# Kernel tuning notes

Hardware: AMD Instinct MI355X
Metric: run time of the kernel (lower is better)

Reference implementation:

```python
import jax, jax.numpy as jnp
import numpy as np

B, S, D, H = 2, 2048, 1024, 16
DH = D // H
NEG = -1000000000.0


def setup_inputs() -> dict:
    key = jax.random.key(0)
    ks = jax.random.split(key, 8)
    q = jax.random.normal(ks[0], (B, S, D), dtype=jnp.float32)
    k = jax.random.normal(ks[1], (B, S, D), dtype=jnp.float32)
    v = jax.random.normal(ks[2], (B, S, D), dtype=jnp.float32)
    # padding mask [B, k_len]; ensure first key position is valid
    mask = jax.random.randint(ks[3], (B, S), 0, 2, dtype=jnp.int32)
    mask = mask.at[:, 0].set(1)
    scale = 1.0 / np.sqrt(D)
    Wq = jax.random.normal(ks[4], (D, D), dtype=jnp.float32) * scale
    Wk = jax.random.normal(ks[5], (D, D), dtype=jnp.float32) * scale
    Wv = jax.random.normal(ks[6], (D, D), dtype=jnp.float32) * scale
    Wo = jax.random.normal(ks[7], (D, D), dtype=jnp.float32) * scale
    return {"q": q, "k": k, "v": v, "mask": mask,
            "Wq": Wq, "Wk": Wk, "Wv": Wv, "Wo": Wo}


def reference(q, k, v, mask, Wq, Wk, Wv, Wo):
    # nn.Linear(bias=False): y = x @ W.T  (W is [out, in])
    Q = jnp.einsum('bsd,ed->bse', q, Wq)
    K = jnp.einsum('bsd,ed->bse', k, Wk)
    V = jnp.einsum('bsd,ed->bse', v, Wv)
    # split heads -> [B, H, S, DH]
    Q = Q.reshape(B, S, H, DH).transpose(0, 2, 1, 3)
    K = K.reshape(B, S, H, DH).transpose(0, 2, 1, 3)
    V = V.reshape(B, S, H, DH).transpose(0, 2, 1, 3)
    scores = jnp.einsum('bhqd,bhkd->bhqk', Q, K) / jnp.float32(np.sqrt(DH))
    # padding mask: [B, K] -> additive [B, 1, 1, K]
    pad = jnp.where(mask == 0, jnp.float32(NEG), jnp.float32(0.0))[:, None, None, :]
    scores = scores + pad
    # causal (mask_future=True): strict upper triangle blocked
    causal = jnp.where(jnp.triu(jnp.ones((S, S), dtype=bool), k=1),
                       jnp.float32(NEG), jnp.float32(0.0))
    scores = scores + causal
    attn = jax.nn.softmax(scores, axis=-1)
    out = jnp.einsum('bhqk,bhkd->bhqd', attn, V)  # [B, H, S, DH]
    out = out.transpose(0, 2, 1, 3).reshape(B, S, D)
    out = jnp.einsum('bsd,ed->bse', out, Wo)
    # dropout: identity in eval mode
    return out
```

## Files before the change

### kernel.cpp

```cpp
#include <hip/hip_runtime.h>
#include <stdint.h>

#define BB 2
#define SS 2048
#define DD 1024
#define HH 16
#define DHH 64

typedef __bf16 bf16_t;
typedef bf16_t bf16x8 __attribute__((ext_vector_type(8)));
typedef float f32x4 __attribute__((ext_vector_type(4)));
typedef short s16x4 __attribute__((ext_vector_type(4)));

union FragU { uint4 u; bf16x8 b; };
union Frag4U { uint2 u; s16x4 s; };

#if __has_builtin(__builtin_amdgcn_exp2f)
#define EXP2(x) __builtin_amdgcn_exp2f(x)
#else
#define EXP2(x) exp2f(x)
#endif

__device__ __forceinline__ unsigned short f2bf(float f) {
  union { float f; unsigned int u; } x; x.f = f;
  unsigned int u = x.u;
  return (unsigned short)((u + 0x7FFFu + ((u >> 16) & 1u)) >> 16);
}

__device__ __forceinline__ uint2 pack4(float4 v) {
  uint2 r;
  r.x = (unsigned)f2bf(v.x) | ((unsigned)f2bf(v.y) << 16);
  r.y = (unsigned)f2bf(v.z) | ((unsigned)f2bf(v.w) << 16);
  return r;
}

__device__ __forceinline__ uint2 packAcc(f32x4 a) {
  uint2 r;
  r.x = (unsigned)f2bf(a[0]) | ((unsigned)f2bf(a[1]) << 16);
  r.y = (unsigned)f2bf(a[2]) | ((unsigned)f2bf(a[3]) << 16);
  return r;
}

__device__ __forceinline__ bf16x8 ldsFrag(const unsigned short* s, int idx) {
  FragU f;
  f.u = *reinterpret_cast<const uint4*>(s + idx);
  return f.b;
}

__device__ __forceinline__ void gload_lds16(const unsigned short* g, unsigned short* s) {
  __builtin_amdgcn_global_load_lds(
      (const __attribute__((address_space(1))) unsigned int*)g,
      (__attribute__((address_space(3))) unsigned int*)s, 16, 0, 0);
}

#define MFMA16(a, b, c) __builtin_amdgcn_mfma_f32_16x16x32_bf16((a), (b), (c), 0, 0, 0)
#define MFMA16K16(a, b, c) __builtin_amdgcn_mfma_f32_16x16x16bf16_1k((a), (b), (c), 0, 0, 0)

__global__ __launch_bounds__(256) void convert_kernel(
    const float* __restrict__ q, const float* __restrict__ k, const float* __restrict__ v,
    const float* __restrict__ Wq, const float* __restrict__ Wk,
    const float* __restrict__ Wv, const float* __restrict__ Wo,
    const int* __restrict__ mask,
    unsigned short* __restrict__ Ab, unsigned short* __restrict__ Wb,
    float* __restrict__ Mf) {
  const int z = blockIdx.y;
  if (z == 7) {
    if (blockIdx.x >= 4) return;
    const size_t base = (size_t)blockIdx.x * 1024 + (size_t)threadIdx.x * 4;
    int4 m4 = *reinterpret_cast<const int4*>(mask + base);
    float4 p;
    p.x = (m4.x == 0) ? -1.0e9f : 0.0f;
    p.y = (m4.y == 0) ? -1.0e9f : 0.0f;
    p.z = (m4.z == 0) ? -1.0e9f : 0.0f;
    p.w = (m4.w == 0) ? -1.0e9f : 0.0f;
    *reinterpret_cast<float4*>(Mf + base) = p;
    return;
  }
  const float* src;
  unsigned short* dst;
  float scale = 1.0f;
  if (z < 3) {
    src = (z == 0) ? q : (z == 1) ? k : v;
    dst = Ab + (size_t)z * BB * SS * DD;
  } else {
    if (blockIdx.x >= (DD * DD / 1024)) return;
    src = (z == 3) ? Wq : (z == 4) ? Wk : (z == 5) ? Wv : Wo;
    dst = Wb + (size_t)(z - 3) * DD * DD;
    if (z == 3) scale = 0.125f * 1.44269504088896f;
  }
  const size_t base = (size_t)blockIdx.x * 1024 + (size_t)threadIdx.x * 4;
  float4 val = *reinterpret_cast<const float4*>(src + base);
  val.x *= scale; val.y *= scale; val.z *= scale; val.w *= scale;
  uint2 p = pack4(val);
  *reinterpret_cast<uint2*>(dst + base) = p;
}

__global__ __launch_bounds__(256) void proj128_kernel(
    const unsigned short* __restrict__ Ab, const unsigned short* __restrict__ Wb,
    unsigned short* __restrict__ Qb, unsigned short* __restrict__ Kb,
    unsigned short* __restrict__ Vt) {
  __shared__ unsigned short sA[2][128 * 64];
  __shared__ unsigned short sB[2][128 * 64];

  const int z = blockIdx.z;
  const unsigned short* A = Ab + (size_t)z * BB * SS * DD;
  const unsigned short* W = Wb + (size_t)z * DD * DD;
  unsigned short* Out = (z == 0) ? Qb : (z == 1) ? Kb : Vt;
  const int layout = (z == 2) ? 1 : 0;

  const int t = threadIdx.x;
  const int lane = t & 63, wave = t >> 6;
  const int quad = lane >> 4, l15 = lane & 15;
  const int wr = wave >> 1, wc = wave & 1;
  const int mBase = blockIdx.x * 128, nBase = blockIdx.y * 128;
  const int srow = lane >> 3, soct = lane & 7;

  f32x4 acc[4][4] = {};

  #pragma unroll
  for (int i = 0; i < 4; ++i) {
    const int g = wave * 4 + i;
    const int row = g * 8 + srow;
    const int oct = soct ^ (row & 7);
    gload_lds16(A + (size_t)(mBase + row) * DD + oct * 8, &sA[0][g * 512]);
    gload_lds16(W + (size_t)(nBase + row) * DD + oct * 8, &sB[0][g * 512]);
  }

  for (int kt = 0; kt < DD / 64; ++kt) {
    __syncthreads();
    if (kt + 1 < DD / 64) {
      const int nb = (kt + 1) & 1;
      const int k1 = (kt + 1) * 64;
      #pragma unroll
      for (int i = 0; i < 4; ++i) {
        const int g = wave * 4 + i;
        const int row = g * 8 + srow;
        const int oct = soct ^ (row & 7);
        gload_lds16(A + (size_t)(mBase + row) * DD + k1 + oct * 8, &sA[nb][g * 512]);
        gload_lds16(W + (size_t)(nBase + row) * DD + k1 + oct * 8, &sB[nb][g * 512]);
      }
    }
    const int cb = kt & 1;
    #pragma unroll
    for (int kk = 0; kk < 2; ++kk) {
      bf16x8 af[4], bfr[4];
      #pragma unroll
      for (int i = 0; i < 4; ++i) {
        const int row = wr * 64 + i * 16 + l15;
        af[i] = ldsFrag(sA[cb], (row * 8 + ((kk * 4 + quad) ^ (l15 & 7))) * 8);
      }
      #pragma unroll
      for (int j = 0; j < 4; ++j) {
        const int row = wc * 64 + j * 16 + l15;
        bfr[j] = ldsFrag(sB[cb], (row * 8 + ((kk * 4 + quad) ^ (l15 & 7))) * 8);
      }
      if (layout == 0) {
        #pragma unroll
        for (int i = 0; i < 4; ++i)
          #pragma unroll
          for (int j = 0; j < 4; ++j)
            acc[i][j] = MFMA16(bfr[j], af[i], acc[i][j]);
      } else {
        #pragma unroll
        for (int i = 0; i < 4; ++i)
          #pragma unroll
          for (int j = 0; j < 4; ++j)
            acc[i][j] = MFMA16(af[i], bfr[j], acc[i][j]);
      }
    }
  }

  const int b = mBase >> 11;
  const int sbase = mBase & (SS - 1);
  if (layout == 0) {
    #pragma unroll
    for (int i = 0; i < 4; ++i) {
      #pragma unroll
      for (int j = 0; j < 4; ++j) {
        const int s = sbase + wr * 64 + i * 16 + l15;
        const int n = nBase + wc * 64 + j * 16 + quad * 4;
        const int h = n >> 6, dh = n & (DHH - 1);
        uint2 w = packAcc(acc[i][j]);
        *reinterpret_cast<uint2*>(
            Out + ((size_t)(b * HH + h) * SS + s) * DHH + dh) = w;
      }
    }
  } else {
    #pragma unroll
    for (int i = 0; i < 4; ++i) {
      #pragma unroll
      for (int j = 0; j < 4; ++j) {
        const int s = sbase + wr * 64 + i * 16 + quad * 4;
        const int n = nBase + wc * 64 + j * 16 + l15;
        const int h = n >> 6, dh = n & (DHH - 1);
        uint2 w = packAcc(acc[i][j]);
        *reinterpret_cast<uint2*>(
            Out + ((size_t)(b * HH + h) * DHH + dh) * SS + s) = w;
      }
    }
  }
}

__global__ __launch_bounds__(256, 4) void attn_kernel(
    const unsigned short* __restrict__ Qb, const unsigned short* __restrict__ Kb,
    const unsigned short* __restrict__ Vt, const float* __restrict__ Mf,
    unsigned short* __restrict__ Obh) {
  __shared__ __align__(16) unsigned short sK[2][64 * 64];
  __shared__ __align__(16) unsigned short sV[2][64 * 64];
  unsigned short* sO = &sK[0][0];

  const int t = threadIdx.x;
  const int lane = t & 63, wave = t >> 6;
  const int quad = lane >> 4, l15 = lane & 15;

  const int id = blockIdx.x;
  const int xcd = id & 7, rest = id >> 3;
  const int hg = rest >> 5;
  const int hd = xcd * 4 + hg;
  const int r5 = rest & 31;
  const int qt = (hg & 1) ? (31 - r5) : r5;
  const int b = hd >> 4;
  const int qb = qt * 64;

  const size_t headOff = (size_t)hd * SS * DHH;
  const unsigned short* Qh = Qb + headOff;
  const unsigned short* Kh = Kb + headOff;
  const unsigned short* Vh = Vt + headOff;
  const float* Mp = Mf + b * SS;

  bf16x8 aq[2];
  {
    const unsigned short* qp = Qh + (size_t)(qb + wave * 16 + l15) * DHH + quad * 8;
    FragU f0, f1;
    f0.u = *reinterpret_cast<const uint4*>(qp);
    f1.u = *reinterpret_cast<const uint4*>(qp + 32);
    aq[0] = f0.b; aq[1] = f1.b;
  }

  const int srow = lane >> 3, soct = lane & 7;

  #pragma unroll
  for (int i = 0; i < 2; ++i) {
    const int g = wave * 2 + i;
    const int row = g * 8 + srow;
    const int oct = soct ^ (row & 7);
    gload_lds16(Kh + (size_t)row * DHH + oct * 8, &sK[0][g * 512]);
    gload_lds16(Vh + (size_t)row * SS + oct * 8, &sV[0][g * 512]);
  }

  float l_lane = 0.0f;
  f32x4 oacc[4] = {};
  const int qrow_abs = qb + wave * 16 + l15;

  for (int c = 0; c <= qt; ++c) {
    __syncthreads();
    if (c < qt) {
      const int c1 = (c + 1) * 64;
      const int nb = (c + 1) & 1;
      #pragma unroll
      for (int i = 0; i < 2; ++i) {
        const int g = wave * 2 + i;
        const int row = g * 8 + srow;
        const int oct = soct ^ (row & 7);
        gload_lds16(Kh + (size_t)(c1 + row) * DHH + oct * 8, &sK[nb][g * 512]);
        gload_lds16(Vh + (size_t)row * SS + c1 + oct * 8, &sV[nb][g * 512]);
      }
    }
    const int cb = c & 1;
    const int c0 = c * 64;

    f32x4 sacc[4] = {};
    #pragma unroll
    for (int kk = 0; kk < 2; ++kk) {
      #pragma unroll
      for (int j = 0; j < 4; ++j) {
        const int row = j * 16 + l15;
        bf16x8 ak = ldsFrag(sK[cb], (row * 8 + ((kk * 4 + quad) ^ (l15 & 7))) * 8);
        sacc[j] = MFMA16(ak, aq[kk], sacc[j]);
      }
    }

    const bool diag = (c == qt);
    s16x4 pk[4];
    #pragma unroll
    for (int j = 0; j < 4; ++j) {
      float4 pf = *reinterpret_cast<const float4*>(Mp + c0 + j * 16 + quad * 4);
      float p0 = EXP2(sacc[j][0] + pf.x);
      float p1 = EXP2(sacc[j][1] + pf.y);
      float p2 = EXP2(sacc[j][2] + pf.z);
      float p3 = EXP2(sacc[j][3] + pf.w);
      if (diag) {
        const int key = c0 + j * 16 + quad * 4;
        p0 = (key + 0 > qrow_abs) ? 0.0f : p0;
        p1 = (key + 1 > qrow_abs) ? 0.0f : p1;
        p2 = (key + 2 > qrow_abs) ? 0.0f : p2;
        p3 = (key + 3 > qrow_abs) ? 0.0f : p3;
      }
      l_lane += (p0 + p1) + (p2 + p3);
      Frag4U fu;
      fu.u.x = __builtin_amdgcn_perm(__float_as_uint(p1) + 0x8000u,
                                     __float_as_uint(p0) + 0x8000u, 0x07060302u);
      fu.u.y = __builtin_amdgcn_perm(__float_as_uint(p3) + 0x8000u,
                                     __float_as_uint(p2) + 0x8000u, 0x07060302u);
      pk[j] = fu.s;
    }

    #pragma unroll
    for (int j = 0; j < 4; ++j) {
      #pragma unroll
      for (int jn = 0; jn < 4; ++jn) {
        const int row = jn * 16 + l15;
        const int oct = (2 * j + (quad >> 1)) ^ (l15 & 7);
        Frag4U av;
        av.u = *reinterpret_cast<const uint2*>(&sV[cb][(row * 8 + oct) * 8 + (quad & 1) * 4]);
        oacc[jn] = MFMA16K16(av.s, pk[j], oacc[jn]);
      }
    }
  }

  float l_l = l_lane + __shfl_xor(l_lane, 16);
  l_l += __shfl_xor(l_l, 32);
  __syncthreads();
  const float inv = 1.0f / l_l;
  #pragma unroll
  for (int jn = 0; jn < 4; ++jn) {
    uint2 w;
    w.x = (unsigned)f2bf(oacc[jn][0] * inv) | ((unsigned)f2bf(oacc[jn][1] * inv) << 16);
    w.y = (unsigned)f2bf(oacc[jn][2] * inv) | ((unsigned)f2bf(oacc[jn][3] * inv) << 16);
    *reinterpret_cast<uint2*>(&sO[(wave * 16 + l15) * 72 + jn * 16 + quad * 4]) = w;
  }
  __syncthreads();
  {
    const int row = t >> 2, seg = t & 3;
    uint4 u0 = *reinterpret_cast<const uint4*>(&sO[row * 72 + seg * 16]);
    uint4 u1 = *reinterpret_cast<const uint4*>(&sO[row * 72 + seg * 16 + 8]);
    unsigned short* dst = Obh + headOff + (size_t)(qb + row) * DHH + seg * 16;
    *reinterpret_cast<uint4*>(dst) = u0;
    *reinterpret_cast<uint4*>(dst + 8) = u1;
  }
}

__global__ __launch_bounds__(256) void outproj_kernel(
    const unsigned short* __restrict__ Obh, const unsigned short* __restrict__ Wb,
    float* __restrict__ Out) {
  __shared__ unsigned short sA[2][128 * 64];
  __shared__ unsigned short sB[2][128 * 64];

  const unsigned short* W = Wb + (size_t)3 * DD * DD;
  const int t = threadIdx.x;
  const int lane = t & 63, wave = t >> 6;
  const int quad = lane >> 4, l15 = lane & 15;
  const int wr = wave >> 1, wc = wave & 1;
  const int mBase = blockIdx.x * 128, nBase = blockIdx.y * 128;
  const int srow = lane >> 3, soct = lane & 7;

  const int bidx = mBase >> 11;
  const int sloc = mBase & (SS - 1);
  const unsigned short* Abase = Obh + (size_t)bidx * HH * SS * DHH;

  f32x4 acc[4][4] = {};

  #pragma unroll
  for (int i = 0; i < 4; ++i) {
    const int g = wave * 4 + i;
    const int row = g * 8 + srow;
    const int oct = soct ^ (row & 7);
    gload_lds16(Abase + ((size_t)0 * SS + sloc + row) * DHH + oct * 8, &sA[0][g * 512]);
    gload_lds16(W + (size_t)(nBase + row) * DD + oct * 8, &sB[0][g * 512]);
  }

  for (int kt = 0; kt < HH; ++kt) {
    __syncthreads();
    if (kt + 1 < HH) {
      const int nb = (kt + 1) & 1;
      #pragma unroll
      for (int i = 0; i < 4; ++i) {
        const int g = wave * 4 + i;
        const int row = g * 8 + srow;
        const int oct = soct ^ (row & 7);
        gload_lds16(Abase + ((size_t)(kt + 1) * SS + sloc + row) * DHH + oct * 8,
                    &sA[nb][g * 512]);
        gload_lds16(W + (size_t)(nBase + row) * DD + (kt + 1) * 64 + oct * 8,
                    &sB[nb][g * 512]);
      }
    }
    const int cb = kt & 1;
    #pragma unroll
    for (int kk = 0; kk < 2; ++kk) {
      bf16x8 af[4], bfr[4];
      #pragma unroll
      for (int i = 0; i < 4; ++i) {
        const int row = wr * 64 + i * 16 + l15;
        af[i] = ldsFrag(sA[cb], (row * 8 + ((kk * 4 + quad) ^ (l15 & 7))) * 8);
      }
      #pragma unroll
      for (int j = 0; j < 4; ++j) {
        const int row = wc * 64 + j * 16 + l15;
        bfr[j] = ldsFrag(sB[cb], (row * 8 + ((kk * 4 + quad) ^ (l15 & 7))) * 8);
      }
      #pragma unroll
      for (int i = 0; i < 4; ++i)
        #pragma unroll
        for (int j = 0; j < 4; ++j)
          acc[i][j] = MFMA16(bfr[j], af[i], acc[i][j]);
    }
  }

  #pragma unroll
  for (int i = 0; i < 4; ++i) {
    #pragma unroll
    for (int j = 0; j < 4; ++j) {
      const int m = mBase + wr * 64 + i * 16 + l15;
      const int n = nBase + wc * 64 + j * 16 + quad * 4;
      float4 w;
      w.x = acc[i][j][0]; w.y = acc[i][j][1];
      w.z = acc[i][j][2]; w.w = acc[i][j][3];
      *reinterpret_cast<float4*>(Out + (size_t)m * DD + n) = w;
    }
  }
}

extern "C" void kernel_launch(void* const* d_in, const int* in_sizes, int n_in,
                              void* d_out, int out_size, void* d_ws, size_t ws_size,
                              hipStream_t stream) {
  (void)in_sizes; (void)n_in; (void)out_size; (void)ws_size;
  const float* q  = (const float*)d_in[0];
  const float* k  = (const float*)d_in[1];
  const float* v  = (const float*)d_in[2];
  const int* mask = (const int*)d_in[3];
  const float* Wq = (const float*)d_in[4];
  const float* Wk = (const float*)d_in[5];
  const float* Wv = (const float*)d_in[6];
  const float* Wo = (const float*)d_in[7];
  float* out = (float*)d_out;

  const size_t AE = (size_t)BB * SS * DD;
  unsigned short* Ab  = (unsigned short*)d_ws;
  unsigned short* Obh = Ab;
  unsigned short* Wb  = Ab + 3 * AE;
  unsigned short* Qb  = Wb + (size_t)4 * DD * DD;
  unsigned short* Kb  = Qb + AE;
  unsigned short* Vt  = Kb + AE;
  float* Mf = (float*)(Vt + AE);

  convert_kernel<<<dim3(AE / 1024, 8), 256, 0, stream>>>(
      q, k, v, Wq, Wk, Wv, Wo, mask, Ab, Wb, Mf);

  proj128_kernel<<<dim3(BB * SS / 128, DD / 128, 3), 256, 0, stream>>>(
      Ab, Wb, Qb, Kb, Vt);

  attn_kernel<<<dim3(32 * HH * BB), 256, 0, stream>>>(Qb, Kb, Vt, Mf, Obh);

  outproj_kernel<<<dim3(BB * SS / 128, DD / 128), 256, 0, stream>>>(Obh, Wb, out);
}
```

Baseline: 224.5 us.

## Process two 64-row query subtiles per attention block to reuse K/V tiles

Each attention block now handles 128 query rows as two 64-row subtiles that share every staged K/V chunk and its LDS fragment loads. This halves the grid and the global K/V traffic per query row. The padding mask row is also preloaded into shared memory instead of being read from global memory per chunk. In exchange, register pressure roughly doubles, occupancy is reduced to 2 blocks per SIMD, fewer blocks are available for load balancing, and the diagonal chunks need special-case masking.

```diff
diff --git a/kernel.cpp b/kernel.cpp
--- a/kernel.cpp
+++ b/kernel.cpp
@@ -201,12 +201,13 @@
   }
 }
 
-__global__ __launch_bounds__(256, 4) void attn_kernel(
+__global__ __launch_bounds__(256, 2) void attn_kernel(
     const unsigned short* __restrict__ Qb, const unsigned short* __restrict__ Kb,
     const unsigned short* __restrict__ Vt, const float* __restrict__ Mf,
     unsigned short* __restrict__ Obh) {
   __shared__ __align__(16) unsigned short sK[2][64 * 64];
   __shared__ __align__(16) unsigned short sV[2][64 * 64];
+  __shared__ __align__(16) float sM[SS];
   unsigned short* sO = &sK[0][0];
 
   const int t = threadIdx.x;
@@ -215,12 +216,12 @@
 
   const int id = blockIdx.x;
   const int xcd = id & 7, rest = id >> 3;
-  const int hg = rest >> 5;
+  const int hg = rest >> 4;
   const int hd = xcd * 4 + hg;
-  const int r5 = rest & 31;
-  const int qt = (hg & 1) ? (31 - r5) : r5;
+  const int r4 = rest & 15;
+  const int qtl = (hg & 2) ? (15 - r4) : r4;
   const int b = hd >> 4;
-  const int qb = qt * 64;
+  const int qb = qtl * 128;
 
   const size_t headOff = (size_t)hd * SS * DHH;
   const unsigned short* Qh = Qb + headOff;
@@ -228,16 +229,25 @@
   const unsigned short* Vh = Vt + headOff;
   const float* Mp = Mf + b * SS;
 
-  bf16x8 aq[2];
-  {
-    const unsigned short* qp = Qh + (size_t)(qb + wave * 16 + l15) * DHH + quad * 8;
+  bf16x8 aq[2][2];
+  #pragma unroll
+  for (int sub = 0; sub < 2; ++sub) {
+    const unsigned short* qp =
+        Qh + (size_t)(qb + sub * 64 + wave * 16 + l15) * DHH + quad * 8;
     FragU f0, f1;
     f0.u = *reinterpret_cast<const uint4*>(qp);
     f1.u = *reinterpret_cast<const uint4*>(qp + 32);
-    aq[0] = f0.b; aq[1] = f1.b;
+    aq[sub][0] = f0.b; aq[sub][1] = f1.b;
   }
 
   const int srow = lane >> 3, soct = lane & 7;
+
+  #pragma unroll
+  for (int i = 0; i < 2; ++i) {
+    const int g = wave * 2 + i;
+    gload_lds16(reinterpret_cast<const unsigned short*>(Mp + g * 256 + lane * 4),
+                reinterpret_cast<unsigned short*>(&sM[g * 256]));
+  }
 
   #pragma unroll
   for (int i = 0; i < 2; ++i) {
@@ -248,95 +258,126 @@
     gload_lds16(Vh + (size_t)row * SS + oct * 8, &sV[0][g * 512]);
   }
 
-  float l_lane = 0.0f;
-  f32x4 oacc[4] = {};
-  const int qrow_abs = qb + wave * 16 + l15;
-
-  for (int c = 0; c <= qt; ++c) {
+  float lsum0 = 0.0f, lsum1 = 0.0f;
+  f32x4 oacc0[4] = {}, oacc1[4] = {};
+  const int qrow0 = qb + wave * 16 + l15;
+  const int qrow1 = qrow0 + 64;
+
+#define QK_SM(SUB, MODE)                                                         \
+  {                                                                              \
+    f32x4 sacc[4] = {};                                                          \
+    _Pragma("unroll")                                                            \
+    for (int kk = 0; kk < 2; ++kk)                                               \
+      _Pragma("unroll")                                                          \
+      for (int j = 0; j < 4; ++j)                                                \
+        sacc[j] = MFMA16(akf[kk][j], aq[SUB][kk], sacc[j]);                      \
+    _Pragma("unroll")                                                            \
+    for (int j = 0; j < 4; ++j) {                                                \
+      float4 pf = *reinterpret_cast<const float4*>(&sM[c0 + j * 16 + quad * 4]); \
+      float p0 = EXP2(sacc[j][0] + pf.x);                                        \
+      float p1 = EXP2(sacc[j][1] + pf.y);                                        \
+      float p2 = EXP2(sacc[j][2] + pf.z);                                        \
+      float p3 = EXP2(sacc[j][3] + pf.w);                                        \
+      if (MODE == 1) {                                                           \
+        const int key = c0 + j * 16 + quad * 4;                                  \
+        p0 = (key + 0 > qrow##SUB) ? 0.0f : p0;                                  \
+        p1 = (key + 1 > qrow##SUB) ? 0.0f : p1;                                  \
+        p2 = (key + 2 > qrow##SUB) ? 0.0f : p2;                                  \
+        p3 = (key + 3 > qrow##SUB) ? 0.0f : p3;                                  \
+      }                                                                          \
+      lsum##SUB += (p0 + p1) + (p2 + p3);                                        \
+      Frag4U fu;                                                                 \
+      fu.u.x = __builtin_amdgcn_perm(__float_as_uint(p1) + 0x8000u,              \
+                                     __float_as_uint(p0) + 0x8000u, 0x07060302u);\
+      fu.u.y = __builtin_amdgcn_perm(__float_as_uint(p3) + 0x8000u,              \
+                                     __float_as_uint(p2) + 0x8000u, 0x07060302u);\
+      pk##SUB[j] = fu.s;                                                         \
+    }                                                                            \
+  }
+
+#define CHUNK(CC, DO_STAGE, M0, M1)                                              \
+  {                                                                              \
+    const int c_ = (CC);                                                         \
+    __syncthreads();                                                             \
+    if (DO_STAGE) {                                                              \
+      const int c1k = (c_ + 1) * 64;                                             \
+      const int nb = (c_ + 1) & 1;                                               \
+      _Pragma("unroll")                                                          \
+      for (int i = 0; i < 2; ++i) {                                              \
+        const int g = wave * 2 + i;                                              \
+        const int row = g * 8 + srow;                                            \
+        const int oct = soct ^ (row & 7);                                        \
+        gload_lds16(Kh + (size_t)(c1k + row) * DHH + oct * 8, &sK[nb][g * 512]); \
+        gload_lds16(Vh + (size_t)row * SS + c1k + oct * 8, &sV[nb][g * 512]);    \
+      }                                                                          \
+    }                                                                            \
+    const int cb = c_ & 1;                                                       \
+    const int c0 = c_ * 64;                                                      \
+    bf16x8 akf[2][4];                                                            \
+    _Pragma("unroll")                                                            \
+    for (int kk = 0; kk < 2; ++kk)                                               \
+      _Pragma("unroll")                                                          \
+      for (int j = 0; j < 4; ++j) {                                              \
+        const int row = j * 16 + l15;                                            \
+        akf[kk][j] =                                                             \
+            ldsFrag(sK[cb], (row * 8 + ((kk * 4 + quad) ^ (l15 & 7))) * 8);      \
+      }                                                                          \
+    s16x4 pk0[4], pk1[4];                                                        \
+    if (M0 != 2) QK_SM(0, M0)                                                    \
+    if (M1 != 2) QK_SM(1, M1)                                                    \
+    _Pragma("unroll")                                                            \
+    for (int j = 0; j < 4; ++j) {                                                \
+      _Pragma("unroll")                                                          \
+      for (int jn = 0; jn < 4; ++jn) {                                           \
+        const int row = jn * 16 + l15;                                           \
+        const int oct = (2 * j + (quad >> 1)) ^ (l15 & 7);                       \
+        Frag4U av;                                                               \
+        av.u = *reinterpret_cast<const uint2*>(                                  \
+            &sV[cb][(row * 8 + oct) * 8 + (quad & 1) * 4]);                      \
+        if (M0 != 2) oacc0[jn] = MFMA16K16(av.s, pk0[j], oacc0[jn]);             \
+        if (M1 != 2) oacc1[jn] = MFMA16K16(av.s, pk1[j], oacc1[jn]);             \
+      }                                                                          \
+    }                                                                            \
+  }
+
+  const int cFull = 2 * qtl;
+  for (int c = 0; c < cFull; ++c) {
+    CHUNK(c, true, 0, 0)
+  }
+  CHUNK(cFull, true, 1, 0)
+  CHUNK(cFull + 1, false, 2, 1)
+
+#undef CHUNK
+#undef QK_SM
+
+  float l0 = lsum0 + __shfl_xor(lsum0, 16);
+  l0 += __shfl_xor(l0, 32);
+  float l1 = lsum1 + __shfl_xor(lsum1, 16);
+  l1 += __shfl_xor(l1, 32);
+  const float inv0 = 1.0f / l0, inv1 = 1.0f / l1;
+
+  #pragma unroll
+  for (int sub = 0; sub < 2; ++sub) {
+    const float inv = sub ? inv1 : inv0;
+    const f32x4* oa = sub ? oacc1 : oacc0;
     __syncthreads();
-    if (c < qt) {
-      const int c1 = (c + 1) * 64;
-      const int nb = (c + 1) & 1;
-      #pragma unroll
-      for (int i = 0; i < 2; ++i) {
-        const int g = wave * 2 + i;
-        const int row = g * 8 + srow;
-        const int oct = soct ^ (row & 7);
-        gload_lds16(Kh + (size_t)(c1 + row) * DHH + oct * 8, &sK[nb][g * 512]);
-        gload_lds16(Vh + (size_t)row * SS + c1 + oct * 8, &sV[nb][g * 512]);
-      }
-    }
-    const int cb = c & 1;
-    const int c0 = c * 64;
-
-    f32x4 sacc[4] = {};
-    #pragma unroll
-    for (int kk = 0; kk < 2; ++kk) {
-      #pragma unroll
-      for (int j = 0; j < 4; ++j) {
-        const int row = j * 16 + l15;
-        bf16x8 ak = ldsFrag(sK[cb], (row * 8 + ((kk * 4 + quad) ^ (l15 & 7))) * 8);
-        sacc[j] = MFMA16(ak, aq[kk], sacc[j]);
-      }
-    }
-
-    const bool diag = (c == qt);
-    s16x4 pk[4];
-    #pragma unroll
-    for (int j = 0; j < 4; ++j) {
-      float4 pf = *reinterpret_cast<const float4*>(Mp + c0 + j * 16 + quad * 4);
-      float p0 = EXP2(sacc[j][0] + pf.x);
-      float p1 = EXP2(sacc[j][1] + pf.y);
-      float p2 = EXP2(sacc[j][2] + pf.z);
-      float p3 = EXP2(sacc[j][3] + pf.w);
-      if (diag) {
-        const int key = c0 + j * 16 + quad * 4;
-        p0 = (key + 0 > qrow_abs) ? 0.0f : p0;
-        p1 = (key + 1 > qrow_abs) ? 0.0f : p1;
-        p2 = (key + 2 > qrow_abs) ? 0.0f : p2;
-        p3 = (key + 3 > qrow_abs) ? 0.0f : p3;
-      }
-      l_lane += (p0 + p1) + (p2 + p3);
-      Frag4U fu;
-      fu.u.x = __builtin_amdgcn_perm(__float_as_uint(p1) + 0x8000u,
-                                     __float_as_uint(p0) + 0x8000u, 0x07060302u);
-      fu.u.y = __builtin_amdgcn_perm(__float_as_uint(p3) + 0x8000u,
-                                     __float_as_uint(p2) + 0x8000u, 0x07060302u);
-      pk[j] = fu.s;
-    }
-
-    #pragma unroll
-    for (int j = 0; j < 4; ++j) {
-      #pragma unroll
-      for (int jn = 0; jn < 4; ++jn) {
-        const int row = jn * 16 + l15;
-        const int oct = (2 * j + (quad >> 1)) ^ (l15 & 7);
-        Frag4U av;
-        av.u = *reinterpret_cast<const uint2*>(&sV[cb][(row * 8 + oct) * 8 + (quad & 1) * 4]);
-        oacc[jn] = MFMA16K16(av.s, pk[j], oacc[jn]);
-      }
-    }
-  }
-
-  float l_l = l_lane + __shfl_xor(l_lane, 16);
-  l_l += __shfl_xor(l_l, 32);
-  __syncthreads();
-  const float inv = 1.0f / l_l;
-  #pragma unroll
-  for (int jn = 0; jn < 4; ++jn) {
-    uint2 w;
-    w.x = (unsigned)f2bf(oacc[jn][0] * inv) | ((unsigned)f2bf(oacc[jn][1] * inv) << 16);
-    w.y = (unsigned)f2bf(oacc[jn][2] * inv) | ((unsigned)f2bf(oacc[jn][3] * inv) << 16);
-    *reinterpret_cast<uint2*>(&sO[(wave * 16 + l15) * 72 + jn * 16 + quad * 4]) = w;
-  }
-  __syncthreads();
-  {
-    const int row = t >> 2, seg = t & 3;
-    uint4 u0 = *reinterpret_cast<const uint4*>(&sO[row * 72 + seg * 16]);
-    uint4 u1 = *reinterpret_cast<const uint4*>(&sO[row * 72 + seg * 16 + 8]);
-    unsigned short* dst = Obh + headOff + (size_t)(qb + row) * DHH + seg * 16;
-    *reinterpret_cast<uint4*>(dst) = u0;
-    *reinterpret_cast<uint4*>(dst + 8) = u1;
+    #pragma unroll
+    for (int jn = 0; jn < 4; ++jn) {
+      uint2 w;
+      w.x = (unsigned)f2bf(oa[jn][0] * inv) | ((unsigned)f2bf(oa[jn][1] * inv) << 16);
+      w.y = (unsigned)f2bf(oa[jn][2] * inv) | ((unsigned)f2bf(oa[jn][3] * inv) << 16);
+      *reinterpret_cast<uint2*>(&sO[(wave * 16 + l15) * 72 + jn * 16 + quad * 4]) = w;
+    }
+    __syncthreads();
+    {
+      const int row = t >> 2, seg = t & 3;
+      uint4 u0 = *reinterpret_cast<const uint4*>(&sO[row * 72 + seg * 16]);
+      uint4 u1 = *reinterpret_cast<const uint4*>(&sO[row * 72 + seg * 16 + 8]);
+      unsigned short* dst =
+          Obh + headOff + (size_t)(qb + sub * 64 + row) * DHH + seg * 16;
+      *reinterpret_cast<uint4*>(dst) = u0;
+      *reinterpret_cast<uint4*>(dst + 8) = u1;
+    }
   }
 }
 
@@ -449,7 +490,7 @@
   proj128_kernel<<<dim3(BB * SS / 128, DD / 128, 3), 256, 0, stream>>>(
       Ab, Wb, Qb, Kb, Vt);
 
-  attn_kernel<<<dim3(32 * HH * BB), 256, 0, stream>>>(Qb, Kb, Vt, Mf, Obh);
+  attn_kernel<<<dim3(16 * HH * BB), 256, 0, stream>>>(Qb, Kb, Vt, Mf, Obh);
 
   outproj_kernel<<<dim3(BB * SS / 128, DD / 128), 256, 0, stream>>>(Obh, Wb, out);
 }
```

New measurement: 224.4 us. About the same (-0.0%).
